# Performance work log

Hardware: AMD Instinct MI355X
Metric: run time of the kernel (lower is better)

The kernel has to match this reference:

```python
import jax, jax.numpy as jnp
import numpy as np

D = 256      # n_feature
LVL = 17     # tree depth (leaf levels)
MIX = 20     # M mixture components


def _lstm_cell(x, h, c, Wih, Whh, bih, bhh):
    # torch.nn.LSTMCell gate order: i, f, g, o
    g = x @ Wih.T + bih + h @ Whh.T + bhh
    i, f, gg, o = jnp.split(g, 4, axis=1)
    c2 = jax.nn.sigmoid(f) * c + jax.nn.sigmoid(i) * jnp.tanh(gg)
    return jax.nn.sigmoid(o) * jnp.tanh(c2), c2


def _get_parameter(y, M):
    parts = jnp.split(y[:, :13 * M], 13, axis=1)
    pi = jax.nn.softmax(parts[0], axis=1)
    mu_x, mu_y = parts[1], parts[2]
    sx, sy = jnp.exp(parts[3]), jnp.exp(parts[4])
    rho_xy = jnp.tanh(parts[5])
    mu_a, mu_b = parts[6], parts[7]
    sa, sb = jnp.exp(parts[8]), jnp.exp(parts[9])
    rho_ab = jnp.tanh(parts[10])
    mu_s, ss = parts[11], jnp.exp(parts[12])
    q = jax.nn.softmax(y[:, -3:], axis=1)
    return (pi, mu_x, mu_y, sx, sy, rho_xy, mu_a, mu_b, sa, sb, rho_ab, mu_s, ss, q)


def _bvn_logpdf(dx, dy, mx, my, sx, sy, rho):
    zx = (dx - mx) / sx
    zy = (dy - my) / sy
    Z = zx ** 2 + zy ** 2 - 2.0 * rho * zx * zy
    return -Z / (2.0 * (1.0 - rho ** 2)) - jnp.log(2.0 * jnp.pi * sx * sy * jnp.sqrt(1.0 - rho ** 2))


def _nll(pt, prm):
    # pt: [n, 8] = (x, y, a, b, slope, p1, p2, p3); prm: GMM parameters, each [n, M]
    pi, mx, my, sx, sy, rxy, ma, mb, sa, sb, rab, ms, ss, q = prm
    lpi = jnp.log(pi)
    dx, dy, da, db, ds = (pt[:, k:k + 1] for k in range(5))
    p = pt[:, 5:8]
    lse = jax.scipy.special.logsumexp
    lxy = lse(lpi + _bvn_logpdf(dx, dy, mx, my, sx, sy, rxy), axis=1)
    lab = lse(lpi + _bvn_logpdf(da, db, ma, mb, sa, sb, rab), axis=1)
    lsl = lse(lpi - (ds - ms) ** 2 / (2.0 * ss ** 2) - jnp.log(jnp.sqrt(2.0 * jnp.pi) * ss), axis=1)
    pen = -(p * jnp.log(q)).sum(axis=1)
    return -(lxy + lab + lsl) + pen


def _expected_pos(prm):
    pi, mx, my, sx, sy, rxy, ma, mb, sa, sb, rab, ms, ss, q = prm
    e = lambda m: (pi * m).sum(axis=1)
    return jnp.concatenate([jnp.stack([e(mx), e(my), e(ma), e(mb), e(ms)], axis=1), q], axis=1)


def _levels(I_flat):
    # I_flat is bottom-up concatenation of per-level [ni,3] blocks of a full binary tree
    n_int = I_flat.shape[0]
    L = int(np.log2(n_int + 1))
    sizes = [2 ** (L - 1 - i) for i in range(L)]
    offs = np.concatenate([[0], np.cumsum(sizes)])
    return [I_flat[offs[i]:offs[i + 1]] for i in range(L)]


def setup_inputs() -> dict:
    key = jax.random.key(0)
    ks = jax.random.split(key, 16)
    N = 2 ** (LVL + 1) - 1  # 262143 total nodes
    # heap-layout full binary tree: children of i are 2i+1, 2i+2; bottom-up levels
    blocks = []
    for l in range(LVL - 1, -1, -1):
        f = np.arange(2 ** l - 1, 2 ** (l + 1) - 1)
        blocks.append(np.stack([2 * f + 1, 2 * f + 2, f], axis=1))
    I_flat = jnp.asarray(np.concatenate(blocks, 0), dtype=jnp.int32)
    s = 0.05
    return {
        "X": jax.random.normal(ks[0], (N, 8), jnp.float32),
        "Feature": jax.random.normal(ks[1], (N, D), jnp.float32),
        "I_flat": I_flat,
        "W_ih_e": jax.random.normal(ks[2], (4 * (D // 2), 8), jnp.float32) * s,
        "W_hh_e": jax.random.normal(ks[3], (4 * (D // 2), D // 2), jnp.float32) * s,
        "b_ih_e": jax.random.normal(ks[4], (4 * (D // 2),), jnp.float32) * s,
        "b_hh_e": jax.random.normal(ks[5], (4 * (D // 2),), jnp.float32) * s,
        "fc_h_W": jax.random.normal(ks[6], (2 * D, D), jnp.float32) * s,
        "fc_h_b": jax.random.normal(ks[7], (2 * D,), jnp.float32) * s,
        "W_ih_d": jax.random.normal(ks[8], (4 * D, D + 8), jnp.float32) * s,
        "W_hh_d": jax.random.normal(ks[9], (4 * D, D), jnp.float32) * s,
        "b_ih_d": jax.random.normal(ks[10], (4 * D,), jnp.float32) * s,
        "b_hh_d": jax.random.normal(ks[11], (4 * D,), jnp.float32) * s,
        "fc_W": jax.random.normal(ks[12], (13 * MIX + 3, D // 2), jnp.float32) * s,
        "fc_b": jax.random.normal(ks[13], (13 * MIX + 3,), jnp.float32) * s,
    }


def reference(X, Feature, I_flat, W_ih_e, W_hh_e, b_ih_e, b_hh_e,
              fc_h_W, fc_h_b, W_ih_d, W_hh_d, b_ih_d, b_hh_d, fc_W, fc_b):
    levels = _levels(I_flat)
    num_I = len(levels)

    # ---- encode: bottom-up gather children -> LSTMCell -> scatter father ----
    Feature_New = Feature
    for I in levels:
        li, ri, fi = I[:, 0], I[:, 1], I[:, 2]
        hl, cl = jnp.split(Feature[li], 2, axis=1)
        hr, cr = jnp.split(Feature[ri], 2, axis=1)
        hlo, clo = _lstm_cell(X[li], hl, cl, W_ih_e, W_hh_e, b_ih_e, b_hh_e)
        hro, cro = _lstm_cell(X[ri], hr, cr, W_ih_e, W_hh_e, b_ih_e, b_hh_e)
        out = jnp.concatenate([hlo + hro, clo + cro], axis=1)
        Feature_New = Feature_New.at[fi].set(out)

    # ---- decode: top-down gather father -> LSTMCell+GMM head -> scatter children ----
    X_P = X
    Feat = Feature_New
    Loss = jnp.float32(0.0)
    for I in reversed(levels):
        li, ri, fi = I[:, 0], I[:, 1], I[:, 2]
        p_l, p_r, p_f = X[li], X[ri], X[fi]
        f_f = Feat[fi]
        z = jnp.tanh(f_f @ fc_h_W.T + fc_h_b)
        h_f, c_f = jnp.split(z, 2, axis=1)
        h_o, c_o = _lstm_cell(jnp.concatenate([p_f, f_f], axis=1), h_f, c_f,
                              W_ih_d, W_hh_d, b_ih_d, b_hh_d)
        h_left, h_right = jnp.split(h_o, 2, axis=1)
        c_left, c_right = jnp.split(c_o, 2, axis=1)
        prm_l = _get_parameter(h_left @ fc_W.T + fc_b, MIX)
        prm_r = _get_parameter(h_right @ fc_W.T + fc_b, MIX)
        direct = _nll(p_l, prm_l) + _nll(p_r, prm_r)
        swapped = _nll(p_l, prm_r) + _nll(p_r, prm_l)
        sw = swapped < direct  # l_r_index == 1 -> swap left/right outputs
        Loss = Loss + jnp.mean(jnp.where(sw, swapped, direct))
        pos_l, pos_r = _expected_pos(prm_l), _expected_pos(prm_r)
        feat_l = jnp.concatenate([h_left, c_left], axis=1)
        feat_r = jnp.concatenate([h_right, c_right], axis=1)
        swc = sw[:, None]
        Feat = Feat.at[li].set(jnp.where(swc, feat_r, feat_l))
        Feat = Feat.at[ri].set(jnp.where(swc, feat_l, feat_r))
        X_P = X_P.at[li].set(jnp.where(swc, pos_r, pos_l))
        X_P = X_P.at[ri].set(jnp.where(swc, pos_l, pos_r))
    return Loss / num_I
```

## Files before the change

### kernel.cpp

```cpp
#include <hip/hip_runtime.h>
#include <hip/hip_bf16.h>
#include <math.h>


#define LOG2PI 1.8378770664093453f

typedef __attribute__((ext_vector_type(8))) short short8;
typedef __attribute__((ext_vector_type(4))) float f32x4;

__device__ inline float sigm(float x) { return 1.0f / (1.0f + expf(-x)); }

__device__ inline ushort f2b(float v) {
    union { float f; unsigned u; } x; x.f = v;
    unsigned r = x.u + 0x7fffu + ((x.u >> 16) & 1u);
    return (ushort)(r >> 16);
}
__device__ inline float b2f(ushort h) {
    union { unsigned u; float f; } x; x.u = ((unsigned)h) << 16; return x.f;
}

__device__ inline void gload16(const void* g, void* l) {
    __builtin_amdgcn_global_load_lds(
        (const __attribute__((address_space(1))) unsigned*)g,
        (__attribute__((address_space(3))) unsigned*)l, 16, 0, 0);
}

template <int ACT, int OUT_MODE>
__global__ __launch_bounds__(256) void gemm_bf16(
    const ushort* __restrict__ A, int lda, int Mclamp,
    const ushort* __restrict__ B, int ldb, int Nclamp,
    const float* __restrict__ bias0, const float* __restrict__ bias1,
    float* __restrict__ Cf, ushort* __restrict__ Cb, int ldc,
    int M, int N, int K)
{
    __shared__ ushort As[128 * 64];
    __shared__ ushort Bs[128 * 64];
    const int tid = threadIdx.x;
    const int lane = tid & 63;
    const int w = tid >> 6;
    const int wr = w >> 1, wc = w & 1;
    const int fr = lane & 15, fq = lane >> 4;
    const int m0 = blockIdx.x * 128, n0 = blockIdx.y * 128;

    f32x4 acc[4][4] = {};

    for (int k0 = 0; k0 < K; k0 += 64) {
        __syncthreads();
        #pragma unroll
        for (int it = 0; it < 4; ++it) {
            const int i = it * 256 + tid;
            const int row = i >> 3, slot = i & 7;
            const int sl = slot ^ (row & 7);
            const int wbase = (i - lane) * 8;
            {
                int gm = m0 + row; gm = gm <= Mclamp ? gm : Mclamp;
                gload16(A + (size_t)gm * lda + k0 + sl * 8, &As[wbase]);
            }
            {
                int gn = n0 + row; gn = gn <= Nclamp ? gn : Nclamp;
                gload16(B + (size_t)gn * ldb + k0 + sl * 8, &Bs[wbase]);
            }
        }
        __syncthreads();
        #pragma unroll
        for (int ks = 0; ks < 2; ++ks) {
            short8 af[4], bfr[4];
            #pragma unroll
            for (int mr = 0; mr < 4; ++mr) {
                const int row = wr * 64 + mr * 16 + fr;
                const int sl = (ks * 4 + fq) ^ (row & 7);
                af[mr] = *(const short8*)&As[row * 64 + sl * 8];
            }
            #pragma unroll
            for (int nc = 0; nc < 4; ++nc) {
                const int row = wc * 64 + nc * 16 + fr;
                const int sl = (ks * 4 + fq) ^ (row & 7);
                bfr[nc] = *(const short8*)&Bs[row * 64 + sl * 8];
            }
            #pragma unroll
            for (int mr = 0; mr < 4; ++mr)
                #pragma unroll
                for (int nc = 0; nc < 4; ++nc)
                    acc[mr][nc] = __builtin_amdgcn_mfma_f32_16x16x32_bf16(
                        af[mr], bfr[nc], acc[mr][nc], 0, 0, 0);
        }
    }

    #pragma unroll
    for (int mr = 0; mr < 4; ++mr) {
        #pragma unroll
        for (int j = 0; j < 4; ++j) {
            const int row = m0 + wr * 64 + mr * 16 + fq * 4 + j;
            if (row >= M) continue;
            #pragma unroll
            for (int nc = 0; nc < 4; ++nc) {
                const int col = n0 + wc * 64 + nc * 16 + fr;
                if (col >= N) continue;
                float v = acc[mr][nc][j] + bias0[col] + (bias1 ? bias1[col] : 0.f);
                if (ACT == 1) v = tanhf(v);
                if (OUT_MODE == 0) Cf[(size_t)row * ldc + col] = v;
                else               Cb[(size_t)row * ldc + col] = f2b(v);
            }
        }
    }
}

__global__ __launch_bounds__(256) void gates_lstm(
    const ushort* __restrict__ Xb,
    const ushort* __restrict__ Fcur,
    const ushort* __restrict__ Zb,
    const ushort* __restrict__ Wg,
    const float*  __restrict__ bg,
    ushort* __restrict__ H, ushort* __restrict__ C, int M)
{
    __shared__ ushort As[128 * 64];
    __shared__ ushort Bs[128 * 64];
    const int tid = threadIdx.x;
    const int lane = tid & 63;
    const int w = tid >> 6;
    const int wr = w >> 1, wc = w & 1;
    const int fr = lane & 15, fq = lane >> 4;
    const int m0 = blockIdx.x * 128, n0 = blockIdx.y * 128;

    f32x4 acc[4][4] = {};

    for (int k0 = 0; k0 < 576; k0 += 64) {
        __syncthreads();
        const int sbase = k0 >> 3;
        #pragma unroll
        for (int it = 0; it < 4; ++it) {
            const int i = it * 256 + tid;
            const int row = i >> 3, slot = i & 7;
            const int sl = slot ^ (row & 7);
            const int wbase = (i - lane) * 8;
            {
                int gm = m0 + row; gm = gm < M ? gm : M - 1;
                const int a = sbase + sl;
                const ushort* src;
                if (a == 0)      src = Xb   + (size_t)gm * 8;
                else if (a < 33) src = Fcur + (size_t)gm * 256 + (size_t)(a - 1) * 8;
                else if (a < 65) src = Zb   + (size_t)gm * 512 + (size_t)(a - 33) * 8;
                else             src = Zb   + (size_t)gm * 512;
                gload16(src, &As[wbase]);
            }
            gload16(Wg + (size_t)(n0 + row) * 576 + k0 + sl * 8, &Bs[wbase]);
        }
        __syncthreads();
        #pragma unroll
        for (int ks = 0; ks < 2; ++ks) {
            short8 af[4], bfr[4];
            #pragma unroll
            for (int mr = 0; mr < 4; ++mr) {
                const int row = wr * 64 + mr * 16 + fr;
                const int sl = (ks * 4 + fq) ^ (row & 7);
                af[mr] = *(const short8*)&As[row * 64 + sl * 8];
            }
            #pragma unroll
            for (int nc = 0; nc < 4; ++nc) {
                const int row = wc * 64 + nc * 16 + fr;
                const int sl = (ks * 4 + fq) ^ (row & 7);
                bfr[nc] = *(const short8*)&Bs[row * 64 + sl * 8];
            }
            #pragma unroll
            for (int mr = 0; mr < 4; ++mr)
                #pragma unroll
                for (int nc = 0; nc < 4; ++nc)
                    acc[mr][nc] = __builtin_amdgcn_mfma_f32_16x16x32_bf16(
                        af[mr], bfr[nc], acc[mr][nc], 0, 0, 0);
        }
    }

    const int q = fr & 3;
    #pragma unroll
    for (int mr = 0; mr < 4; ++mr) {
        const int node = m0 + wr * 64 + mr * 16 + fq * 4 + q;
        #pragma unroll
        for (int nc = 0; nc < 4; ++nc) {
            const int col = n0 + wc * 64 + nc * 16 + fr;
            f32x4 v = acc[mr][nc];
            const float b = bg[col];
            v[0] += b; v[1] += b; v[2] += b; v[3] += b;
            float gv[4];
            gv[q] = v[q];
            #pragma unroll
            for (int m = 1; m < 4; ++m)
                gv[q ^ m] = __shfl_xor(v[q ^ m], m);
            if (node < M) {
                const int t = (col >> 2) & 255;
                const float cf = b2f(Zb[(size_t)node * 512 + 256 + t]);
                const float c2 = sigm(gv[1]) * cf + sigm(gv[0]) * tanhf(gv[2]);
                const float hv = sigm(gv[3]) * tanhf(c2);
                H[(size_t)node * 256 + t] = f2b(hv);
                C[(size_t)node * 256 + t] = f2b(c2);
            }
        }
    }
}

__global__ __launch_bounds__(256) void conv_f2b(const float* __restrict__ s,
                                                ushort* __restrict__ d, int n)
{
    int i = blockIdx.x * 256 + threadIdx.x;
    if (i < n) d[i] = f2b(s[i]);
}
__global__ __launch_bounds__(256) void pack_wg(const float* __restrict__ Wih,
                                               const float* __restrict__ Whh,
                                               ushort* __restrict__ d)
{
    int i = blockIdx.x * 256 + threadIdx.x;
    if (i >= 1024 * 576) return;
    int np = i / 576, c = i % 576;
    int n = (np & 3) * 256 + (np >> 2);
    float v = 0.f;
    if (c < 264) v = Wih[n * 264 + c];
    else if (c < 520) v = Whh[n * 256 + (c - 264)];
    d[i] = f2b(v);
}
__global__ __launch_bounds__(256) void pack_bg(const float* __restrict__ bih,
                                               const float* __restrict__ bhh,
                                               float* __restrict__ d)
{
    int np = blockIdx.x * 256 + threadIdx.x;
    if (np >= 1024) return;
    int n = (np & 3) * 256 + (np >> 2);
    d[np] = bih[n] + bhh[n];
}
__global__ __launch_bounds__(256) void pack_wy(const float* __restrict__ W,
                                               ushort* __restrict__ d)
{
    int i = blockIdx.x * 256 + threadIdx.x;
    if (i >= 320 * 128) return;
    int r = i / 128;
    d[i] = f2b(r < 263 ? W[i] : 0.f);
}

__global__ __launch_bounds__(256) void encoder_root(
    const float* __restrict__ X, const float* __restrict__ Feature,
    const float* __restrict__ Wih, const float* __restrict__ Whh,
    const float* __restrict__ bih, const float* __restrict__ bhh,
    ushort* __restrict__ Fcur0)
{
    __shared__ float gsh[2][512];
    __shared__ float hc[2][256];
    const int t = threadIdx.x;
    for (int ch = 0; ch < 2; ++ch) {
        const int node = 1 + ch;
        const float* x = X + node * 8;
        const float* h = Feature + (size_t)node * 256;
        #pragma unroll
        for (int gi = 0; gi < 2; ++gi) {
            int g = t + gi * 256;
            float s = bih[g] + bhh[g];
            const float* wi = Wih + (size_t)g * 8;
            #pragma unroll
            for (int k = 0; k < 8; ++k) s += wi[k] * x[k];
            const float* wh = Whh + (size_t)g * 128;
            for (int k = 0; k < 128; ++k) s += wh[k] * h[k];
            gsh[ch][g] = s;
        }
    }
    __syncthreads();
    {
        int ch = t >> 7, u = t & 127;
        float i_ = gsh[ch][u], f_ = gsh[ch][128 + u];
        float gg = gsh[ch][256 + u], o_ = gsh[ch][384 + u];
        float c = Feature[(size_t)(1 + ch) * 256 + 128 + u];
        float c2 = sigm(f_) * c + sigm(i_) * tanhf(gg);
        hc[ch][u] = sigm(o_) * tanhf(c2);
        hc[ch][128 + u] = c2;
    }
    __syncthreads();
    Fcur0[t] = f2b(hc[0][t] + hc[1][t]);
}

__device__ inline float halfmax(float v) {
    #pragma unroll
    for (int o = 16; o >= 1; o >>= 1) v = fmaxf(v, __shfl_xor(v, o));
    return v;
}
__device__ inline float halfsum(float v) {
    #pragma unroll
    for (int o = 16; o >= 1; o >>= 1) v += __shfl_xor(v, o);
    return v;
}
__device__ inline float lse20(float t) {
    float m = halfmax(t);
    float s = halfsum(expf(t - m));
    return m + logf(s);
}

__global__ __launch_bounds__(256) void ynll(
    const ushort* __restrict__ Hb, const ushort* __restrict__ Cc,
    const ushort* __restrict__ Wyp,
    const float* __restrict__ fc_b, const float* __restrict__ X,
    ushort* __restrict__ FeatNext, float* __restrict__ loss,
    int Bc, long long nb, int j0, float scale, int writeFeat)
{
    __shared__ ushort Hs[32 * 128];
    __shared__ float Ys[32][324];
    __shared__ float lsum[4];
    const int tid = threadIdx.x;
    const int lane = tid & 63;
    const int wv = tid >> 6;
    const int fr = lane & 15, fq = lane >> 4;
    const int n16 = blockIdx.x * 16;

    #pragma unroll
    for (int it = 0; it < 2; ++it) {
        const int i = it * 256 + tid;
        const int row = i >> 4, slot = i & 15;
        const int sl = slot ^ (row & 7);
        int gr = n16 * 2 + row;
        const int grmax = 2 * Bc - 1;
        gr = gr <= grmax ? gr : grmax;
        gload16(Hb + (size_t)gr * 128 + sl * 8, &Hs[(i - lane) * 8]);
    }
    __syncthreads();

    f32x4 acc[2][5] = {};
    #pragma unroll
    for (int ks = 0; ks < 4; ++ks) {
        short8 a[2];
        #pragma unroll
        for (int rf = 0; rf < 2; ++rf) {
            const int row = rf * 16 + fr;
            const int sl = (ks * 4 + fq) ^ (row & 7);
            a[rf] = *(const short8*)&Hs[row * 128 + sl * 8];
        }
        #pragma unroll
        for (int n = 0; n < 5; ++n) {
            const short8 b = *(const short8*)(
                Wyp + (size_t)(wv * 80 + n * 16 + fr) * 128 + ks * 32 + fq * 8);
            acc[0][n] = __builtin_amdgcn_mfma_f32_16x16x32_bf16(a[0], b, acc[0][n], 0, 0, 0);
            acc[1][n] = __builtin_amdgcn_mfma_f32_16x16x32_bf16(a[1], b, acc[1][n], 0, 0, 0);
        }
    }
    #pragma unroll
    for (int rf = 0; rf < 2; ++rf)
        #pragma unroll
        for (int n = 0; n < 5; ++n)
            #pragma unroll
            for (int j = 0; j < 4; ++j) {
                const int row = rf * 16 + fq * 4 + j;
                const int col = wv * 80 + n * 16 + fr;
                Ys[row][col] = acc[rf][n][j] + (col < 263 ? fc_b[col] : 0.f);
            }
    __syncthreads();

    float wsum = 0.f;
    const int half = lane >> 5, k = lane & 31;
    #pragma unroll
    for (int s4 = 0; s4 < 4; ++s4) {
        const int jj = wv * 4 + s4;
        const int j = n16 + jj;
        if (j >= Bc) break;
        const float* yb = Ys[2 * jj + half];
        float v = (k < 20) ? yb[k] : -INFINITY;
        float mm = halfmax(v);
        float se = halfsum((k < 20) ? expf(v - mm) : 0.f);
        float lpi = v - mm - logf(se);
        float mx = 0, my = 0, sx = 1, sy = 1, rho = 0, omr = 1, cxy = 0;
        float ma = 0, mb2 = 0, sa = 1, sb = 1, rab = 0, omr2 = 1, cab = 0;
        float ms = 0, ss2 = 1, csl = 0;
        if (k < 20) {
            mx = yb[20 + k]; my = yb[40 + k];
            float lsx = yb[60 + k], lsy = yb[80 + k];
            sx = expf(lsx); sy = expf(lsy);
            rho = tanhf(yb[100 + k]); omr = 1.f - rho * rho;
            cxy = LOG2PI + lsx + lsy + 0.5f * logf(omr);
            ma = yb[120 + k]; mb2 = yb[140 + k];
            float lsa = yb[160 + k], lsb = yb[180 + k];
            sa = expf(lsa); sb = expf(lsb);
            rab = tanhf(yb[200 + k]); omr2 = 1.f - rab * rab;
            cab = LOG2PI + lsa + lsb + 0.5f * logf(omr2);
            ms = yb[220 + k]; float lss = yb[240 + k];
            ss2 = expf(lss);
            csl = 0.5f * LOG2PI + lss;
        }
        float lq0, lq1, lq2;
        {
            float q0 = yb[260], q1 = yb[261], q2 = yb[262];
            float qm = fmaxf(q0, fmaxf(q1, q2));
            float l = logf(expf(q0 - qm) + expf(q1 - qm) + expf(q2 - qm)) + qm;
            lq0 = q0 - l; lq1 = q1 - l; lq2 = q2 - l;
        }
        const long long fi = nb + j0 + j;
        const float* pl = X + (size_t)(2 * fi + 1) * 8;
        const float* pr = X + (size_t)(2 * fi + 2) * 8;
        float res[2];
        #pragma unroll
        for (int s = 0; s < 2; ++s) {
            const float* pt = s ? pr : pl;
            float dx = pt[0], dy = pt[1], da = pt[2], db = pt[3], ds = pt[4];
            float t1 = -INFINITY, t2 = -INFINITY, t3 = -INFINITY;
            if (k < 20) {
                float zx = (dx - mx) / sx, zy = (dy - my) / sy;
                float Zz = zx * zx + zy * zy - 2.f * rho * zx * zy;
                t1 = lpi - Zz / (2.f * omr) - cxy;
                float za = (da - ma) / sa, zb = (db - mb2) / sb;
                float Z2 = za * za + zb * zb - 2.f * rab * za * zb;
                t2 = lpi - Z2 / (2.f * omr2) - cab;
                float zs = ds - ms;
                t3 = lpi - (zs * zs) / (2.f * ss2 * ss2) - csl;
            }
            float l1 = lse20(t1), l2 = lse20(t2), l3 = lse20(t3);
            float pen = -(pt[5] * lq0 + pt[6] * lq1 + pt[7] * lq2);
            res[s] = -(l1 + l2 + l3) + pen;
        }
        float Aval = half ? res[1] : res[0];
        float Bval = half ? res[0] : res[1];
        float direct = Aval + __shfl_xor(Aval, 32);
        float swapped = Bval + __shfl_xor(Bval, 32);
        bool sw = swapped < direct;
        wsum += sw ? swapped : direct;
        if (writeFeat) {
            const size_t Jg = 2 * (size_t)(j0 + j);
            const ushort* Hj = Hb + (size_t)j * 256;
            const ushort* Cj = Cc + (size_t)j * 256;
            const int offL = sw ? 128 : 0;
            const int offR = 128 - offL;
            const int part = lane >> 5;
            const int c = (lane & 31) * 4;
            ushort4 vL = *(const ushort4*)((part ? Cj : Hj) + offL + c);
            ushort4 vR = *(const ushort4*)((part ? Cj : Hj) + offR + c);
            *(ushort4*)(FeatNext + Jg * 256 + part * 128 + c) = vL;
            *(ushort4*)(FeatNext + (Jg + 1) * 256 + part * 128 + c) = vR;
        }
    }
    if (lane == 0) lsum[wv] = wsum;
    __syncthreads();
    if (tid == 0)
        atomicAdd(loss, (lsum[0] + lsum[1] + lsum[2] + lsum[3]) * scale);
}

extern "C" void kernel_launch(void* const* d_in, const int* in_sizes, int n_in,
                              void* d_out, int out_size, void* d_ws, size_t ws_size,
                              hipStream_t stream)
{
    const float* X       = (const float*)d_in[0];
    const float* Feature = (const float*)d_in[1];
    const float* W_ih_e  = (const float*)d_in[3];
    const float* W_hh_e  = (const float*)d_in[4];
    const float* b_ih_e  = (const float*)d_in[5];
    const float* b_hh_e  = (const float*)d_in[6];
    const float* fc_h_W  = (const float*)d_in[7];
    const float* fc_h_b  = (const float*)d_in[8];
    const float* W_ih_d  = (const float*)d_in[9];
    const float* W_hh_d  = (const float*)d_in[10];
    const float* b_ih_d  = (const float*)d_in[11];
    const float* b_hh_d  = (const float*)d_in[12];
    const float* fc_W    = (const float*)d_in[13];
    const float* fc_b    = (const float*)d_in[14];
    const int Nnodes = in_sizes[0] / 8;

    float* out = (float*)d_out;
    hipMemsetAsync(d_out, 0, sizeof(float), stream);

    char* cur = (char*)d_ws;
    auto take = [&](size_t bytes) {
        char* p = cur;
        cur += (bytes + 255) & ~(size_t)255;
        return p;
    };
    ushort* featA = (ushort*)take((size_t)65536 * 256 * 2);
    ushort* featB = (ushort*)take((size_t)32768 * 256 * 2);
    ushort* Wz    = (ushort*)take((size_t)512 * 256 * 2);
    ushort* Wg    = (ushort*)take((size_t)1024 * 576 * 2);
    ushort* Wy    = (ushort*)take((size_t)320 * 128 * 2);
    float*  bg    = (float*) take((size_t)1024 * 4);
    ushort* Xb    = (ushort*)take((size_t)Nnodes * 8 * 2);
    const size_t fixed_used = (size_t)(cur - (char*)d_ws);
    int CB = 65536;
    while (CB > 2048 && fixed_used + (size_t)CB * 2048 + 4096 > ws_size) CB >>= 1;
    ushort* Zb = (ushort*)take((size_t)CB * 512 * 2);
    ushort* Hb = (ushort*)take((size_t)CB * 256 * 2);
    ushort* Cc = (ushort*)take((size_t)CB * 256 * 2);

    conv_f2b<<<(512 * 256 + 255) / 256, 256, 0, stream>>>(fc_h_W, Wz, 512 * 256);
    pack_wg<<<(1024 * 576 + 255) / 256, 256, 0, stream>>>(W_ih_d, W_hh_d, Wg);
    pack_bg<<<4, 256, 0, stream>>>(b_ih_d, b_hh_d, bg);
    pack_wy<<<(320 * 128 + 255) / 256, 256, 0, stream>>>(fc_W, Wy);
    conv_f2b<<<(Nnodes * 8 + 255) / 256, 256, 0, stream>>>(X, Xb, Nnodes * 8);

    encoder_root<<<1, 256, 0, stream>>>(X, Feature, W_ih_e, W_hh_e, b_ih_e, b_hh_e, featA);

    for (int l = 0; l < 17; ++l) {
        const int B = 1 << l;
        const long long nb = B - 1;
        ushort* Fcur  = (l & 1) ? featB : featA;
        ushort* Fnext = (l & 1) ? featA : featB;
        const int writeFeat = (l < 16) ? 1 : 0;
        const float scale = 1.f / ((float)B * 17.f);
        for (int j0 = 0; j0 < B; j0 += CB) {
            const int Bc = (B - j0 < CB) ? (B - j0) : CB;
            const int mg = (Bc + 127) / 128;
            gemm_bf16<1, 1><<<dim3(mg, 4), 256, 0, stream>>>(
                Fcur + (size_t)j0 * 256, 256, Bc - 1,
                Wz, 256, 511,
                fc_h_b, nullptr, nullptr, Zb, 512, Bc, 512, 256);
            gates_lstm<<<dim3(mg, 8), 256, 0, stream>>>(
                Xb + (size_t)(nb + j0) * 8,
                Fcur + (size_t)j0 * 256,
                Zb, Wg, bg, Hb, Cc, Bc);
            ynll<<<(Bc + 15) / 16, 256, 0, stream>>>(
                Hb, Cc, Wy, fc_b, X,
                writeFeat ? Fnext : nullptr, out,
                Bc, nb, j0, scale, writeFeat);
        }
    }
}
```

Measured before the change: 1.463 ms.

## Fuse first six tree levels into one persistent block and merge packing kernels

Levels 0-5 of the decoder are now processed inside a single one-block kernel that performs the Z GEMM, gate GEMM with LSTM, and output/NLL per level in shared memory. This replaces 18 small launches that each used very few blocks. The five weight-packing kernels are merged into one launch, and the GEMM K loop is templated so it can be unrolled. The single-block kernel serializes the small levels on one CU, and the minimum chunk size is raised.

```diff
diff --git a/kernel.cpp b/kernel.cpp
--- a/kernel.cpp
+++ b/kernel.cpp
@@ -25,13 +25,110 @@
         (__attribute__((address_space(3))) unsigned*)l, 16, 0, 0);
 }
 
-template <int ACT, int OUT_MODE>
+__device__ inline f32x4 mfma16(short8 a, short8 b, f32x4 c) {
+    return __builtin_amdgcn_mfma_f32_16x16x32_bf16(a, b, c, 0, 0, 0);
+}
+
+__device__ inline float halfmax(float v) {
+    #pragma unroll
+    for (int o = 16; o >= 1; o >>= 1) v = fmaxf(v, __shfl_xor(v, o));
+    return v;
+}
+__device__ inline float halfsum(float v) {
+    #pragma unroll
+    for (int o = 16; o >= 1; o >>= 1) v += __shfl_xor(v, o);
+    return v;
+}
+__device__ inline float lse20(float t) {
+    float m = halfmax(t);
+    float s = halfsum(expf(t - m));
+    return m + logf(s);
+}
+
+__device__ inline float nll_node(const float* yb, const float* X,
+                                 long long fi, int lane, bool& sw_out)
+{
+    const int half = lane >> 5, k = lane & 31;
+    float v = (k < 20) ? yb[k] : -INFINITY;
+    float mm = halfmax(v);
+    float se = halfsum((k < 20) ? expf(v - mm) : 0.f);
+    float lpi = v - mm - logf(se);
+    float mx = 0, my = 0, sx = 1, sy = 1, rho = 0, omr = 1, cxy = 0;
+    float ma = 0, mb2 = 0, sa = 1, sb = 1, rab = 0, omr2 = 1, cab = 0;
+    float ms = 0, ss2 = 1, csl = 0;
+    if (k < 20) {
+        mx = yb[20 + k]; my = yb[40 + k];
+        float lsx = yb[60 + k], lsy = yb[80 + k];
+        sx = expf(lsx); sy = expf(lsy);
+        rho = tanhf(yb[100 + k]); omr = 1.f - rho * rho;
+        cxy = LOG2PI + lsx + lsy + 0.5f * logf(omr);
+        ma = yb[120 + k]; mb2 = yb[140 + k];
+        float lsa = yb[160 + k], lsb = yb[180 + k];
+        sa = expf(lsa); sb = expf(lsb);
+        rab = tanhf(yb[200 + k]); omr2 = 1.f - rab * rab;
+        cab = LOG2PI + lsa + lsb + 0.5f * logf(omr2);
+        ms = yb[220 + k]; float lss = yb[240 + k];
+        ss2 = expf(lss);
+        csl = 0.5f * LOG2PI + lss;
+    }
+    float lq0, lq1, lq2;
+    {
+        float q0 = yb[260], q1 = yb[261], q2 = yb[262];
+        float qm = fmaxf(q0, fmaxf(q1, q2));
+        float l = logf(expf(q0 - qm) + expf(q1 - qm) + expf(q2 - qm)) + qm;
+        lq0 = q0 - l; lq1 = q1 - l; lq2 = q2 - l;
+    }
+    const float* pl = X + (size_t)(2 * fi + 1) * 8;
+    const float* pr = X + (size_t)(2 * fi + 2) * 8;
+    float res[2];
+    #pragma unroll
+    for (int s = 0; s < 2; ++s) {
+        const float* pt = s ? pr : pl;
+        float dx = pt[0], dy = pt[1], da = pt[2], db = pt[3], ds = pt[4];
+        float t1 = -INFINITY, t2 = -INFINITY, t3 = -INFINITY;
+        if (k < 20) {
+            float zx = (dx - mx) / sx, zy = (dy - my) / sy;
+            float Zz = zx * zx + zy * zy - 2.f * rho * zx * zy;
+            t1 = lpi - Zz / (2.f * omr) - cxy;
+            float za = (da - ma) / sa, zb = (db - mb2) / sb;
+            float Z2 = za * za + zb * zb - 2.f * rab * za * zb;
+            t2 = lpi - Z2 / (2.f * omr2) - cab;
+            float zs = ds - ms;
+            t3 = lpi - (zs * zs) / (2.f * ss2 * ss2) - csl;
+        }
+        float l1 = lse20(t1), l2 = lse20(t2), l3 = lse20(t3);
+        float pen = -(pt[5] * lq0 + pt[6] * lq1 + pt[7] * lq2);
+        res[s] = -(l1 + l2 + l3) + pen;
+    }
+    float Aval = half ? res[1] : res[0];
+    float Bval = half ? res[0] : res[1];
+    float direct = Aval + __shfl_xor(Aval, 32);
+    float swapped = Bval + __shfl_xor(Bval, 32);
+    sw_out = swapped < direct;
+    return sw_out ? swapped : direct;
+}
+
+__device__ inline void feat_write(ushort* FeatNext, const ushort* Hj,
+                                  const ushort* Cj, long long j, bool sw, int lane)
+{
+    const size_t Jg = 2 * (size_t)j;
+    const int offL = sw ? 128 : 0;
+    const int offR = 128 - offL;
+    const int part = lane >> 5;
+    const int c = (lane & 31) * 4;
+    ushort4 vL = *(const ushort4*)((part ? Cj : Hj) + offL + c);
+    ushort4 vR = *(const ushort4*)((part ? Cj : Hj) + offR + c);
+    *(ushort4*)(FeatNext + Jg * 256 + part * 128 + c) = vL;
+    *(ushort4*)(FeatNext + (Jg + 1) * 256 + part * 128 + c) = vR;
+}
+
+template <int ACT, int OUT_MODE, int KK>
 __global__ __launch_bounds__(256) void gemm_bf16(
     const ushort* __restrict__ A, int lda, int Mclamp,
     const ushort* __restrict__ B, int ldb, int Nclamp,
-    const float* __restrict__ bias0, const float* __restrict__ bias1,
+    const float* __restrict__ bias0,
     float* __restrict__ Cf, ushort* __restrict__ Cb, int ldc,
-    int M, int N, int K)
+    int M, int N)
 {
     __shared__ ushort As[128 * 64];
     __shared__ ushort Bs[128 * 64];
@@ -44,7 +141,8 @@
 
     f32x4 acc[4][4] = {};
 
-    for (int k0 = 0; k0 < K; k0 += 64) {
+    #pragma unroll
+    for (int k0 = 0; k0 < KK; k0 += 64) {
         __syncthreads();
         #pragma unroll
         for (int it = 0; it < 4; ++it) {
@@ -81,8 +179,7 @@
             for (int mr = 0; mr < 4; ++mr)
                 #pragma unroll
                 for (int nc = 0; nc < 4; ++nc)
-                    acc[mr][nc] = __builtin_amdgcn_mfma_f32_16x16x32_bf16(
-                        af[mr], bfr[nc], acc[mr][nc], 0, 0, 0);
+                    acc[mr][nc] = mfma16(af[mr], bfr[nc], acc[mr][nc]);
         }
     }
 
@@ -96,7 +193,7 @@
             for (int nc = 0; nc < 4; ++nc) {
                 const int col = n0 + wc * 64 + nc * 16 + fr;
                 if (col >= N) continue;
-                float v = acc[mr][nc][j] + bias0[col] + (bias1 ? bias1[col] : 0.f);
+                float v = acc[mr][nc][j] + bias0[col];
                 if (ACT == 1) v = tanhf(v);
                 if (OUT_MODE == 0) Cf[(size_t)row * ldc + col] = v;
                 else               Cb[(size_t)row * ldc + col] = f2b(v);
@@ -124,6 +221,7 @@
 
     f32x4 acc[4][4] = {};
 
+    #pragma unroll
     for (int k0 = 0; k0 < 576; k0 += 64) {
         __syncthreads();
         const int sbase = k0 >> 3;
@@ -165,8 +263,7 @@
             for (int mr = 0; mr < 4; ++mr)
                 #pragma unroll
                 for (int nc = 0; nc < 4; ++nc)
-                    acc[mr][nc] = __builtin_amdgcn_mfma_f32_16x16x32_bf16(
-                        af[mr], bfr[nc], acc[mr][nc], 0, 0, 0);
+                    acc[mr][nc] = mfma16(af[mr], bfr[nc], acc[mr][nc]);
         }
     }
 
@@ -197,41 +294,117 @@
     }
 }
 
-__global__ __launch_bounds__(256) void conv_f2b(const float* __restrict__ s,
-                                                ushort* __restrict__ d, int n)
+__global__ __launch_bounds__(256) void ynll(
+    const ushort* __restrict__ Hb, const ushort* __restrict__ Cc,
+    const ushort* __restrict__ Wyp,
+    const float* __restrict__ fc_b, const float* __restrict__ X,
+    ushort* __restrict__ FeatNext, float* __restrict__ loss,
+    int Bc, long long nb_fi, float scale, int writeFeat)
+{
+    __shared__ ushort Hs[32 * 128];
+    __shared__ float Ys[32][324];
+    __shared__ float lsum[4];
+    const int tid = threadIdx.x;
+    const int lane = tid & 63;
+    const int wv = tid >> 6;
+    const int fr = lane & 15, fq = lane >> 4;
+    const int n16 = blockIdx.x * 16;
+
+    #pragma unroll
+    for (int it = 0; it < 2; ++it) {
+        const int i = it * 256 + tid;
+        const int row = i >> 4, slot = i & 15;
+        const int sl = slot ^ (row & 7);
+        int gr = n16 * 2 + row;
+        const int grmax = 2 * Bc - 1;
+        gr = gr <= grmax ? gr : grmax;
+        gload16(Hb + (size_t)gr * 128 + sl * 8, &Hs[(i - lane) * 8]);
+    }
+    __syncthreads();
+
+    f32x4 acc[2][5] = {};
+    #pragma unroll
+    for (int ks = 0; ks < 4; ++ks) {
+        short8 a[2];
+        #pragma unroll
+        for (int rf = 0; rf < 2; ++rf) {
+            const int row = rf * 16 + fr;
+            const int sl = (ks * 4 + fq) ^ (row & 7);
+            a[rf] = *(const short8*)&Hs[row * 128 + sl * 8];
+        }
+        #pragma unroll
+        for (int n = 0; n < 5; ++n) {
+            const short8 b = *(const short8*)(
+                Wyp + (size_t)(wv * 80 + n * 16 + fr) * 128 + ks * 32 + fq * 8);
+            acc[0][n] = mfma16(a[0], b, acc[0][n]);
+            acc[1][n] = mfma16(a[1], b, acc[1][n]);
+        }
+    }
+    #pragma unroll
+    for (int rf = 0; rf < 2; ++rf)
+        #pragma unroll
+        for (int n = 0; n < 5; ++n)
+            #pragma unroll
+            for (int j = 0; j < 4; ++j) {
+                const int row = rf * 16 + fq * 4 + j;
+                const int col = wv * 80 + n * 16 + fr;
+                Ys[row][col] = acc[rf][n][j] + (col < 263 ? fc_b[col] : 0.f);
+            }
+    __syncthreads();
+
+    float wsum = 0.f;
+    #pragma unroll
+    for (int s4 = 0; s4 < 4; ++s4) {
+        const int jj = wv * 4 + s4;
+        const int j = n16 + jj;
+        if (j >= Bc) break;
+        bool sw;
+        wsum += nll_node(Ys[2 * jj + (lane >> 5)], X, nb_fi + j, lane, sw);
+        if (writeFeat)
+            feat_write(FeatNext, Hb + (size_t)j * 256, Cc + (size_t)j * 256,
+                       j, sw, lane);
+    }
+    if (lane == 0) lsum[wv] = wsum;
+    __syncthreads();
+    if (tid == 0)
+        atomicAdd(loss, (lsum[0] + lsum[1] + lsum[2] + lsum[3]) * scale);
+}
+
+__global__ __launch_bounds__(256) void pack_all(
+    const float* __restrict__ fc_h_W, ushort* __restrict__ Wz,
+    const float* __restrict__ Wih, const float* __restrict__ Whh,
+    ushort* __restrict__ Wg,
+    const float* __restrict__ bih, const float* __restrict__ bhh,
+    float* __restrict__ bg,
+    const float* __restrict__ fcW, ushort* __restrict__ Wy,
+    const float* __restrict__ X, ushort* __restrict__ Xb, int nx)
 {
     int i = blockIdx.x * 256 + threadIdx.x;
-    if (i < n) d[i] = f2b(s[i]);
-}
-__global__ __launch_bounds__(256) void pack_wg(const float* __restrict__ Wih,
-                                               const float* __restrict__ Whh,
-                                               ushort* __restrict__ d)
-{
-    int i = blockIdx.x * 256 + threadIdx.x;
-    if (i >= 1024 * 576) return;
-    int np = i / 576, c = i % 576;
-    int n = (np & 3) * 256 + (np >> 2);
-    float v = 0.f;
-    if (c < 264) v = Wih[n * 264 + c];
-    else if (c < 520) v = Whh[n * 256 + (c - 264)];
-    d[i] = f2b(v);
-}
-__global__ __launch_bounds__(256) void pack_bg(const float* __restrict__ bih,
-                                               const float* __restrict__ bhh,
-                                               float* __restrict__ d)
-{
-    int np = blockIdx.x * 256 + threadIdx.x;
-    if (np >= 1024) return;
-    int n = (np & 3) * 256 + (np >> 2);
-    d[np] = bih[n] + bhh[n];
-}
-__global__ __launch_bounds__(256) void pack_wy(const float* __restrict__ W,
-                                               ushort* __restrict__ d)
-{
-    int i = blockIdx.x * 256 + threadIdx.x;
-    if (i >= 320 * 128) return;
-    int r = i / 128;
-    d[i] = f2b(r < 263 ? W[i] : 0.f);
+    if (i < 131072) { Wz[i] = f2b(fc_h_W[i]); return; }
+    i -= 131072;
+    if (i < 589824) {
+        int np = i / 576, c = i - np * 576;
+        int n = (np & 3) * 256 + (np >> 2);
+        float v = 0.f;
+        if (c < 264) v = Wih[n * 264 + c];
+        else if (c < 520) v = Whh[n * 256 + (c - 264)];
+        Wg[i] = f2b(v);
+        return;
+    }
+    i -= 589824;
+    if (i < 1024) {
+        int n = (i & 3) * 256 + (i >> 2);
+        bg[i] = bih[n] + bhh[n];
+        return;
+    }
+    i -= 1024;
+    if (i < 40960) {
+        int r = i / 128;
+        Wy[i] = f2b(r < 263 ? fcW[i] : 0.f);
+        return;
+    }
+    i -= 40960;
+    if (i < nx) Xb[i] = f2b(X[i]);
 }
 
 __global__ __launch_bounds__(256) void encoder_root(
@@ -273,164 +446,190 @@
     Fcur0[t] = f2b(hc[0][t] + hc[1][t]);
 }
 
-__device__ inline float halfmax(float v) {
-    #pragma unroll
-    for (int o = 16; o >= 1; o >>= 1) v = fmaxf(v, __shfl_xor(v, o));
-    return v;
-}
-__device__ inline float halfsum(float v) {
-    #pragma unroll
-    for (int o = 16; o >= 1; o >>= 1) v += __shfl_xor(v, o);
-    return v;
-}
-__device__ inline float lse20(float t) {
-    float m = halfmax(t);
-    float s = halfsum(expf(t - m));
-    return m + logf(s);
-}
-
-__global__ __launch_bounds__(256) void ynll(
-    const ushort* __restrict__ Hb, const ushort* __restrict__ Cc,
-    const ushort* __restrict__ Wyp,
-    const float* __restrict__ fc_b, const float* __restrict__ X,
-    ushort* __restrict__ FeatNext, float* __restrict__ loss,
-    int Bc, long long nb, int j0, float scale, int writeFeat)
-{
-    __shared__ ushort Hs[32 * 128];
-    __shared__ float Ys[32][324];
+__global__ __launch_bounds__(256) void small_levels(
+    const float* __restrict__ X, const ushort* __restrict__ Xb,
+    ushort* __restrict__ featA, ushort* __restrict__ featB,
+    const ushort* __restrict__ Wz, const float* __restrict__ fc_h_b,
+    const ushort* __restrict__ Wg, const float* __restrict__ bg,
+    const ushort* __restrict__ Wyp, const float* __restrict__ fc_b,
+    ushort* __restrict__ Hb, ushort* __restrict__ Cc,
+    float* __restrict__ loss)
+{
+    __shared__ char pool[53248] __attribute__((aligned(16)));
     __shared__ float lsum[4];
+    ushort* Asm = (ushort*)pool;
+    ushort* Zc  = (ushort*)(pool + 36864);
+    ushort* Hs  = (ushort*)pool;
+    float (*Ys)[324] = (float (*)[324])(pool + 8192);
+
     const int tid = threadIdx.x;
     const int lane = tid & 63;
-    const int wv = tid >> 6;
+    const int wv  = tid >> 6;
     const int fr = lane & 15, fq = lane >> 4;
-    const int n16 = blockIdx.x * 16;
-
-    #pragma unroll
-    for (int it = 0; it < 2; ++it) {
-        const int i = it * 256 + tid;
-        const int row = i >> 4, slot = i & 15;
-        const int sl = slot ^ (row & 7);
-        int gr = n16 * 2 + row;
-        const int grmax = 2 * Bc - 1;
-        gr = gr <= grmax ? gr : grmax;
-        gload16(Hb + (size_t)gr * 128 + sl * 8, &Hs[(i - lane) * 8]);
-    }
-    __syncthreads();
-
-    f32x4 acc[2][5] = {};
-    #pragma unroll
-    for (int ks = 0; ks < 4; ++ks) {
-        short8 a[2];
-        #pragma unroll
-        for (int rf = 0; rf < 2; ++rf) {
-            const int row = rf * 16 + fr;
-            const int sl = (ks * 4 + fq) ^ (row & 7);
-            a[rf] = *(const short8*)&Hs[row * 128 + sl * 8];
-        }
-        #pragma unroll
-        for (int n = 0; n < 5; ++n) {
-            const short8 b = *(const short8*)(
-                Wyp + (size_t)(wv * 80 + n * 16 + fr) * 128 + ks * 32 + fq * 8);
-            acc[0][n] = __builtin_amdgcn_mfma_f32_16x16x32_bf16(a[0], b, acc[0][n], 0, 0, 0);
-            acc[1][n] = __builtin_amdgcn_mfma_f32_16x16x32_bf16(a[1], b, acc[1][n], 0, 0, 0);
-        }
-    }
-    #pragma unroll
-    for (int rf = 0; rf < 2; ++rf)
-        #pragma unroll
-        for (int n = 0; n < 5; ++n)
-            #pragma unroll
-            for (int j = 0; j < 4; ++j) {
-                const int row = rf * 16 + fq * 4 + j;
-                const int col = wv * 80 + n * 16 + fr;
-                Ys[row][col] = acc[rf][n][j] + (col < 263 ? fc_b[col] : 0.f);
-            }
-    __syncthreads();
-
-    float wsum = 0.f;
-    const int half = lane >> 5, k = lane & 31;
-    #pragma unroll
-    for (int s4 = 0; s4 < 4; ++s4) {
-        const int jj = wv * 4 + s4;
-        const int j = n16 + jj;
-        if (j >= Bc) break;
-        const float* yb = Ys[2 * jj + half];
-        float v = (k < 20) ? yb[k] : -INFINITY;
-        float mm = halfmax(v);
-        float se = halfsum((k < 20) ? expf(v - mm) : 0.f);
-        float lpi = v - mm - logf(se);
-        float mx = 0, my = 0, sx = 1, sy = 1, rho = 0, omr = 1, cxy = 0;
-        float ma = 0, mb2 = 0, sa = 1, sb = 1, rab = 0, omr2 = 1, cab = 0;
-        float ms = 0, ss2 = 1, csl = 0;
-        if (k < 20) {
-            mx = yb[20 + k]; my = yb[40 + k];
-            float lsx = yb[60 + k], lsy = yb[80 + k];
-            sx = expf(lsx); sy = expf(lsy);
-            rho = tanhf(yb[100 + k]); omr = 1.f - rho * rho;
-            cxy = LOG2PI + lsx + lsy + 0.5f * logf(omr);
-            ma = yb[120 + k]; mb2 = yb[140 + k];
-            float lsa = yb[160 + k], lsb = yb[180 + k];
-            sa = expf(lsa); sb = expf(lsb);
-            rab = tanhf(yb[200 + k]); omr2 = 1.f - rab * rab;
-            cab = LOG2PI + lsa + lsb + 0.5f * logf(omr2);
-            ms = yb[220 + k]; float lss = yb[240 + k];
-            ss2 = expf(lss);
-            csl = 0.5f * LOG2PI + lss;
-        }
-        float lq0, lq1, lq2;
+
+    for (int l = 0; l <= 5; ++l) {
+        const int B = 1 << l;
+        const long long nb = B - 1;
+        ushort* Fcur  = (l & 1) ? featB : featA;
+        ushort* Fnext = (l & 1) ? featA : featB;
+        const float scale = 1.f / ((float)B * 17.f);
+
+        for (int c = tid; c < 1280; c += 256) {
+            const int r = c / 40, s5 = c - r * 40;
+            const int s = s5 < 33 ? s5 : s5 + 32;
+            const int ss = s ^ (r & 7);
+            short8 v = {0, 0, 0, 0, 0, 0, 0, 0};
+            if (s == 0)
+                v = *(const short8*)(Xb + (size_t)(nb + r) * 8);
+            else if (s < 33)
+                v = *(const short8*)(Fcur + (size_t)r * 256 + (s - 1) * 8);
+            *(short8*)&Asm[r * 576 + ss * 8] = v;
+        }
+        __syncthreads();
         {
-            float q0 = yb[260], q1 = yb[261], q2 = yb[262];
-            float qm = fmaxf(q0, fmaxf(q1, q2));
-            float l = logf(expf(q0 - qm) + expf(q1 - qm) + expf(q2 - qm)) + qm;
-            lq0 = q0 - l; lq1 = q1 - l; lq2 = q2 - l;
-        }
-        const long long fi = nb + j0 + j;
-        const float* pl = X + (size_t)(2 * fi + 1) * 8;
-        const float* pr = X + (size_t)(2 * fi + 2) * 8;
-        float res[2];
-        #pragma unroll
-        for (int s = 0; s < 2; ++s) {
-            const float* pt = s ? pr : pl;
-            float dx = pt[0], dy = pt[1], da = pt[2], db = pt[3], ds = pt[4];
-            float t1 = -INFINITY, t2 = -INFINITY, t3 = -INFINITY;
-            if (k < 20) {
-                float zx = (dx - mx) / sx, zy = (dy - my) / sy;
-                float Zz = zx * zx + zy * zy - 2.f * rho * zx * zy;
-                t1 = lpi - Zz / (2.f * omr) - cxy;
-                float za = (da - ma) / sa, zb = (db - mb2) / sb;
-                float Z2 = za * za + zb * zb - 2.f * rab * za * zb;
-                t2 = lpi - Z2 / (2.f * omr2) - cab;
-                float zs = ds - ms;
-                t3 = lpi - (zs * zs) / (2.f * ss2 * ss2) - csl;
-            }
-            float l1 = lse20(t1), l2 = lse20(t2), l3 = lse20(t3);
-            float pen = -(pt[5] * lq0 + pt[6] * lq1 + pt[7] * lq2);
-            res[s] = -(l1 + l2 + l3) + pen;
-        }
-        float Aval = half ? res[1] : res[0];
-        float Bval = half ? res[0] : res[1];
-        float direct = Aval + __shfl_xor(Aval, 32);
-        float swapped = Bval + __shfl_xor(Bval, 32);
-        bool sw = swapped < direct;
-        wsum += sw ? swapped : direct;
-        if (writeFeat) {
-            const size_t Jg = 2 * (size_t)(j0 + j);
-            const ushort* Hj = Hb + (size_t)j * 256;
-            const ushort* Cj = Cc + (size_t)j * 256;
-            const int offL = sw ? 128 : 0;
-            const int offR = 128 - offL;
-            const int part = lane >> 5;
-            const int c = (lane & 31) * 4;
-            ushort4 vL = *(const ushort4*)((part ? Cj : Hj) + offL + c);
-            ushort4 vR = *(const ushort4*)((part ? Cj : Hj) + offR + c);
-            *(ushort4*)(FeatNext + Jg * 256 + part * 128 + c) = vL;
-            *(ushort4*)(FeatNext + (Jg + 1) * 256 + part * 128 + c) = vR;
-        }
-    }
-    if (lane == 0) lsum[wv] = wsum;
-    __syncthreads();
-    if (tid == 0)
-        atomicAdd(loss, (lsum[0] + lsum[1] + lsum[2] + lsum[3]) * scale);
+            f32x4 acc[2][8] = {};
+            for (int ks = 0; ks < 8; ++ks) {
+                short8 a[2];
+                #pragma unroll
+                for (int mf = 0; mf < 2; ++mf) {
+                    const int r = mf * 16 + fr;
+                    const int ss = (1 + ks * 4 + fq) ^ (r & 7);
+                    a[mf] = *(const short8*)&Asm[r * 576 + ss * 8];
+                }
+                #pragma unroll
+                for (int nf = 0; nf < 8; ++nf) {
+                    const short8 b = *(const short8*)(
+                        Wz + (size_t)(wv * 128 + nf * 16 + fr) * 256 + ks * 32 + fq * 8);
+                    acc[0][nf] = mfma16(a[0], b, acc[0][nf]);
+                    acc[1][nf] = mfma16(a[1], b, acc[1][nf]);
+                }
+            }
+            #pragma unroll
+            for (int mf = 0; mf < 2; ++mf)
+                #pragma unroll
+                for (int nf = 0; nf < 8; ++nf)
+                    #pragma unroll
+                    for (int j = 0; j < 4; ++j) {
+                        const int r = mf * 16 + fq * 4 + j;
+                        const int col = wv * 128 + nf * 16 + fr;
+                        const float z = tanhf(acc[mf][nf][j] + fc_h_b[col]);
+                        if (col < 256) {
+                            const int ss = (33 + (col >> 3)) ^ (r & 7);
+                            Asm[r * 576 + ss * 8 + (col & 7)] = f2b(z);
+                        } else {
+                            Zc[r * 256 + (col - 256)] = f2b(z);
+                        }
+                    }
+        }
+        __syncthreads();
+        for (int p = 0; p < 2; ++p) {
+            f32x4 acc[2][8] = {};
+            const int cbase = wv * 256 + p * 128;
+            for (int ks = 0; ks < 18; ++ks) {
+                short8 a[2];
+                #pragma unroll
+                for (int mf = 0; mf < 2; ++mf) {
+                    const int r = mf * 16 + fr;
+                    const int ss = (ks * 4 + fq) ^ (r & 7);
+                    a[mf] = *(const short8*)&Asm[r * 576 + ss * 8];
+                }
+                #pragma unroll
+                for (int nf = 0; nf < 8; ++nf) {
+                    const short8 b = *(const short8*)(
+                        Wg + (size_t)(cbase + nf * 16 + fr) * 576 + ks * 32 + fq * 8);
+                    acc[0][nf] = mfma16(a[0], b, acc[0][nf]);
+                    acc[1][nf] = mfma16(a[1], b, acc[1][nf]);
+                }
+            }
+            const int q = fr & 3;
+            #pragma unroll
+            for (int mf = 0; mf < 2; ++mf) {
+                const int r = mf * 16 + fq * 4 + q;
+                #pragma unroll
+                for (int nf = 0; nf < 8; ++nf) {
+                    const int col = cbase + nf * 16 + fr;
+                    f32x4 v = acc[mf][nf];
+                    const float bb = bg[col];
+                    v[0] += bb; v[1] += bb; v[2] += bb; v[3] += bb;
+                    float gv[4];
+                    gv[q] = v[q];
+                    #pragma unroll
+                    for (int m = 1; m < 4; ++m)
+                        gv[q ^ m] = __shfl_xor(v[q ^ m], m);
+                    if (r < B) {
+                        const int t = col >> 2;
+                        const float cf = b2f(Zc[r * 256 + t]);
+                        const float c2 = sigm(gv[1]) * cf + sigm(gv[0]) * tanhf(gv[2]);
+                        const float hv = sigm(gv[3]) * tanhf(c2);
+                        Hb[(size_t)r * 256 + t] = f2b(hv);
+                        Cc[(size_t)r * 256 + t] = f2b(c2);
+                    }
+                }
+            }
+        }
+        __syncthreads();
+        for (int sub = 0; sub < 2; ++sub) {
+            const int n16 = sub * 16;
+            if (n16 < B) {
+                #pragma unroll
+                for (int it = 0; it < 2; ++it) {
+                    const int i = it * 256 + tid;
+                    const int row = i >> 4, slot = i & 15;
+                    const int sl = slot ^ (row & 7);
+                    int gr = n16 * 2 + row;
+                    const int grmax = 2 * B - 1;
+                    gr = gr <= grmax ? gr : grmax;
+                    gload16(Hb + (size_t)gr * 128 + sl * 8, &Hs[(i - lane) * 8]);
+                }
+                __syncthreads();
+                f32x4 acc[2][5] = {};
+                #pragma unroll
+                for (int ks = 0; ks < 4; ++ks) {
+                    short8 a[2];
+                    #pragma unroll
+                    for (int rf = 0; rf < 2; ++rf) {
+                        const int row = rf * 16 + fr;
+                        const int sl = (ks * 4 + fq) ^ (row & 7);
+                        a[rf] = *(const short8*)&Hs[row * 128 + sl * 8];
+                    }
+                    #pragma unroll
+                    for (int n = 0; n < 5; ++n) {
+                        const short8 b = *(const short8*)(
+                            Wyp + (size_t)(wv * 80 + n * 16 + fr) * 128 + ks * 32 + fq * 8);
+                        acc[0][n] = mfma16(a[0], b, acc[0][n]);
+                        acc[1][n] = mfma16(a[1], b, acc[1][n]);
+                    }
+                }
+                #pragma unroll
+                for (int rf = 0; rf < 2; ++rf)
+                    #pragma unroll
+                    for (int n = 0; n < 5; ++n)
+                        #pragma unroll
+                        for (int j = 0; j < 4; ++j) {
+                            const int row = rf * 16 + fq * 4 + j;
+                            const int col = wv * 80 + n * 16 + fr;
+                            Ys[row][col] = acc[rf][n][j] + (col < 263 ? fc_b[col] : 0.f);
+                        }
+                __syncthreads();
+                float wsum = 0.f;
+                #pragma unroll
+                for (int s4 = 0; s4 < 4; ++s4) {
+                    const int jj = wv * 4 + s4;
+                    const int j = n16 + jj;
+                    if (j >= B) break;
+                    bool sw;
+                    wsum += nll_node(Ys[2 * jj + (lane >> 5)], X, nb + j, lane, sw);
+                    feat_write(Fnext, Hb + (size_t)j * 256, Cc + (size_t)j * 256,
+                               j, sw, lane);
+                }
+                if (lane == 0) lsum[wv] = wsum;
+                __syncthreads();
+                if (tid == 0)
+                    atomicAdd(loss, (lsum[0] + lsum[1] + lsum[2] + lsum[3]) * scale);
+                __syncthreads();
+            }
+        }
+    }
 }
 
 extern "C" void kernel_launch(void* const* d_in, const int* in_sizes, int n_in,
@@ -471,20 +670,22 @@
     ushort* Xb    = (ushort*)take((size_t)Nnodes * 8 * 2);
     const size_t fixed_used = (size_t)(cur - (char*)d_ws);
     int CB = 65536;
-    while (CB > 2048 && fixed_used + (size_t)CB * 2048 + 4096 > ws_size) CB >>= 1;
+    while (CB > 8192 && fixed_used + (size_t)CB * 2048 + 4096 > ws_size) CB >>= 1;
     ushort* Zb = (ushort*)take((size_t)CB * 512 * 2);
     ushort* Hb = (ushort*)take((size_t)CB * 256 * 2);
     ushort* Cc = (ushort*)take((size_t)CB * 256 * 2);
 
-    conv_f2b<<<(512 * 256 + 255) / 256, 256, 0, stream>>>(fc_h_W, Wz, 512 * 256);
-    pack_wg<<<(1024 * 576 + 255) / 256, 256, 0, stream>>>(W_ih_d, W_hh_d, Wg);
-    pack_bg<<<4, 256, 0, stream>>>(b_ih_d, b_hh_d, bg);
-    pack_wy<<<(320 * 128 + 255) / 256, 256, 0, stream>>>(fc_W, Wy);
-    conv_f2b<<<(Nnodes * 8 + 255) / 256, 256, 0, stream>>>(X, Xb, Nnodes * 8);
+    const int nx = Nnodes * 8;
+    const int packTotal = 131072 + 589824 + 1024 + 40960 + nx;
+    pack_all<<<(packTotal + 255) / 256, 256, 0, stream>>>(
+        fc_h_W, Wz, W_ih_d, W_hh_d, Wg, b_ih_d, b_hh_d, bg, fc_W, Wy, X, Xb, nx);
 
     encoder_root<<<1, 256, 0, stream>>>(X, Feature, W_ih_e, W_hh_e, b_ih_e, b_hh_e, featA);
 
-    for (int l = 0; l < 17; ++l) {
+    small_levels<<<1, 256, 0, stream>>>(
+        X, Xb, featA, featB, Wz, fc_h_b, Wg, bg, Wy, fc_b, Hb, Cc, out);
+
+    for (int l = 6; l < 17; ++l) {
         const int B = 1 << l;
         const long long nb = B - 1;
         ushort* Fcur  = (l & 1) ? featB : featA;
@@ -494,18 +695,18 @@
         for (int j0 = 0; j0 < B; j0 += CB) {
             const int Bc = (B - j0 < CB) ? (B - j0) : CB;
             const int mg = (Bc + 127) / 128;
-            gemm_bf16<1, 1><<<dim3(mg, 4), 256, 0, stream>>>(
+            gemm_bf16<1, 1, 256><<<dim3(mg, 4), 256, 0, stream>>>(
                 Fcur + (size_t)j0 * 256, 256, Bc - 1,
                 Wz, 256, 511,
-                fc_h_b, nullptr, nullptr, Zb, 512, Bc, 512, 256);
+                fc_h_b, nullptr, Zb, 512, Bc, 512);
             gates_lstm<<<dim3(mg, 8), 256, 0, stream>>>(
                 Xb + (size_t)(nb + j0) * 8,
                 Fcur + (size_t)j0 * 256,
                 Zb, Wg, bg, Hb, Cc, Bc);
             ynll<<<(Bc + 15) / 16, 256, 0, stream>>>(
                 Hb, Cc, Wy, fc_b, X,
-                writeFeat ? Fnext : nullptr, out,
-                Bc, nb, j0, scale, writeFeat);
-        }
-    }
-}
+                (writeFeat ? Fnext + (size_t)2 * j0 * 256 : (ushort*)nullptr), out,
+                Bc, nb + j0, scale, writeFeat);
+        }
+    }
+}
```

Measured after the change: 1.778 ms. +21.5%, slower.
